# Kernel tuning notes

Measured on AMD Instinct MI355X. Metric: run time of the kernel, lower is better.

Reference implementation:

```python
import jax, jax.numpy as jnp
import numpy as np

KERNEL_SIZES = (3, 7, 15, 31)


def setup_inputs() -> dict:
    key = jax.random.key(0)
    x = jax.random.normal(key, (16, 4096, 512), dtype=jnp.float32)
    kernel_weights = jnp.ones((len(KERNEL_SIZES),), dtype=jnp.float32) / len(KERNEL_SIZES)
    return {"x": x, "kernel_weights": kernel_weights}


def _box_avg(xc, k):
    # xc: [B, F, S] channels-first; replicate-pad then depthwise box filter of width k
    B, Fc, S = xc.shape
    p = k // 2
    xp = jnp.pad(xc, ((0, 0), (0, 0), (p, p)), mode='edge')
    kern = jnp.full((Fc, 1, k), 1.0 / k, dtype=xc.dtype)  # depthwise: O=F, I/groups=1
    return jax.lax.conv_general_dilated(
        xp, kern, window_strides=(1,), padding='VALID',
        dimension_numbers=('NCW', 'OIW', 'NCW'), feature_group_count=Fc)


def reference(x, kernel_weights):
    # x: [B, S, F]
    w = jax.nn.softmax(kernel_weights)  # softmax over the 4 scales
    xc = jnp.transpose(x, (0, 2, 1))    # [B, F, S]
    out = jnp.zeros_like(xc)
    for i, k in enumerate(KERNEL_SIZES):
        out = out + w[i] * _box_avg(xc, k)
    return jnp.transpose(out, (0, 2, 1))  # [B, S, F]
```

## Files before the change

### kernel.cpp

```cpp
#include <hip/hip_runtime.h>
#include <math.h>

constexpr int B = 16;
constexpr int S = 4096;
constexpr int F = 512;
constexpr int L = 64;
constexpr int BLOCK = 256;

__global__ __launch_bounds__(BLOCK) void msavg_kernel(
    const float* __restrict__ x, const float* __restrict__ kw,
    float* __restrict__ out) {
  const int f  = blockIdx.x * BLOCK + threadIdx.x;
  const int t0 = blockIdx.y * L;
  const int b  = blockIdx.z;

  float w0 = kw[0], w1 = kw[1], w2 = kw[2], w3 = kw[3];
  float m  = fmaxf(fmaxf(w0, w1), fmaxf(w2, w3));
  float e0 = expf(w0 - m), e1 = expf(w1 - m), e2 = expf(w2 - m), e3 = expf(w3 - m);
  float inv = 1.0f / (e0 + e1 + e2 + e3);
  const float c3  = e0 * inv * (1.0f / 3.0f);
  const float c7  = e1 * inv * (1.0f / 7.0f);
  const float c15 = e2 * inv * (1.0f / 15.0f);
  const float c31 = e3 * inv * (1.0f / 31.0f);

  const float* xb = x   + ((size_t)b * S) * F + f;
  float*       ob = out + ((size_t)b * S) * F + f;

  float prev[32], cur[32];

  {
    float p = 0.0f;
#pragma unroll
    for (int j = 0; j < 32; ++j) {
      int s = t0 - 16 + j;
      s = s < 0 ? 0 : (s > S - 1 ? S - 1 : s);
      p += xb[(size_t)s * F];
      prev[j] = p;
    }
  }

#pragma unroll
  for (int g = 0; g < L / 32; ++g) {
    const int T = t0 + g * 32;

    float xv[32];
    if (T + 47 <= S - 1) {
#pragma unroll
      for (int j = 0; j < 32; ++j) xv[j] = xb[(size_t)(T + 16 + j) * F];
    } else {
#pragma unroll
      for (int j = 0; j < 32; ++j) {
        int s = T + 16 + j;
        s = s > S - 1 ? S - 1 : s;
        xv[j] = xb[(size_t)s * F];
      }
    }

    {
      float p = prev[31];
#pragma unroll
      for (int j = 0; j < 32; ++j) {
        p += xv[j];
        cur[j] = p;
      }
    }

#pragma unroll
    for (int j = 0; j < 32; ++j) {
      float Pp15 = (j < 1)  ? prev[j + 31] : cur[j - 1];
      float Pp7  = (j < 9)  ? prev[j + 23] : cur[j - 9];
      float Pp3  = (j < 13) ? prev[j + 19] : cur[j - 13];
      float Pp1  = (j < 15) ? prev[j + 17] : cur[j - 15];
      float Pm2  = (j < 18) ? prev[j + 14] : cur[j - 18];
      float Pm4  = (j < 20) ? prev[j + 12] : cur[j - 20];
      float Pm8  = (j < 24) ? prev[j + 8]  : cur[j - 24];
      float Pm16 = prev[j];
      float o = c3  * (Pp1  - Pm2) +
                c7  * (Pp3  - Pm4) +
                c15 * (Pp7  - Pm8) +
                c31 * (Pp15 - Pm16);
      ob[(size_t)(T + j) * F] = o;
    }

#pragma unroll
    for (int j = 0; j < 32; ++j) prev[j] = cur[j];
  }
}

extern "C" void kernel_launch(void* const* d_in, const int* in_sizes, int n_in,
                              void* d_out, int out_size, void* d_ws, size_t ws_size,
                              hipStream_t stream) {
  const float* x  = (const float*)d_in[0];
  const float* kw = (const float*)d_in[1];
  float* out = (float*)d_out;
  (void)in_sizes; (void)n_in; (void)out_size; (void)d_ws; (void)ws_size;

  dim3 grid(F / BLOCK, S / L, B);
  msavg_kernel<<<grid, BLOCK, 0, stream>>>(x, kw, out);
}
```

Before: 238.0 us.

## Vectorize to float2 per thread, shrink prefix window groups, add occupancy bound

Each thread now handles two adjacent feature columns using float2 vector loads and stores, and uses packed float2 arithmetic. The sliding prefix-sum window moves in 16-row groups (four groups per block) instead of 32-row groups, so fewer registers are live at once, and launch_bounds requests 4 blocks per CU. The goal is wider memory transactions and higher occupancy on this bandwidth-bound stencil. The cost is half as many blocks along F, which cuts the total thread count, and a larger register footprint per element pair that could limit the requested occupancy.

Result: slower. 265.6 us (+11.6%).

```diff
diff --git a/kernel.cpp b/kernel.cpp
--- a/kernel.cpp
+++ b/kernel.cpp
@@ -4,15 +4,20 @@
 constexpr int B = 16;
 constexpr int S = 4096;
 constexpr int F = 512;
-constexpr int L = 64;
+constexpr int G = 16;
+constexpr int NG = 4;
+constexpr int L = G * NG;
 constexpr int BLOCK = 256;
 
-__global__ __launch_bounds__(BLOCK) void msavg_kernel(
+typedef float v2f __attribute__((ext_vector_type(2)));
+static __device__ __forceinline__ v2f vs(float s) { return (v2f){s, s}; }
+
+__global__ __launch_bounds__(BLOCK, 4) void msavg_kernel(
     const float* __restrict__ x, const float* __restrict__ kw,
     float* __restrict__ out) {
-  const int f  = blockIdx.x * BLOCK + threadIdx.x;
-  const int t0 = blockIdx.y * L;
-  const int b  = blockIdx.z;
+  const int fpair = blockIdx.x * BLOCK + threadIdx.x;
+  const int t0    = blockIdx.y * L;
+  const int b     = blockIdx.z;
 
   float w0 = kw[0], w1 = kw[1], w2 = kw[2], w3 = kw[3];
   float m  = fmaxf(fmaxf(w0, w1), fmaxf(w2, w3));
@@ -23,67 +28,70 @@
   const float c15 = e2 * inv * (1.0f / 15.0f);
   const float c31 = e3 * inv * (1.0f / 31.0f);
 
-  const float* xb = x   + ((size_t)b * S) * F + f;
-  float*       ob = out + ((size_t)b * S) * F + f;
+  constexpr int RS = F / 2;
+  const v2f* xb = (const v2f*)(x   + ((size_t)b * S) * F) + fpair;
+  v2f*       ob = (v2f*)      (out + ((size_t)b * S) * F) + fpair;
 
-  float prev[32], cur[32];
-
+  v2f prev[32];
   {
-    float p = 0.0f;
+    v2f p = vs(0.0f);
 #pragma unroll
     for (int j = 0; j < 32; ++j) {
       int s = t0 - 16 + j;
       s = s < 0 ? 0 : (s > S - 1 ? S - 1 : s);
-      p += xb[(size_t)s * F];
+      p += xb[(size_t)s * RS];
       prev[j] = p;
     }
   }
 
 #pragma unroll
-  for (int g = 0; g < L / 32; ++g) {
-    const int T = t0 + g * 32;
+  for (int g = 0; g < NG; ++g) {
+    const int T = t0 + g * G;
 
-    float xv[32];
-    if (T + 47 <= S - 1) {
+    v2f xv[G];
+    if (T + 16 + G - 1 <= S - 1) {
 #pragma unroll
-      for (int j = 0; j < 32; ++j) xv[j] = xb[(size_t)(T + 16 + j) * F];
+      for (int j = 0; j < G; ++j) xv[j] = xb[(size_t)(T + 16 + j) * RS];
     } else {
 #pragma unroll
-      for (int j = 0; j < 32; ++j) {
+      for (int j = 0; j < G; ++j) {
         int s = T + 16 + j;
         s = s > S - 1 ? S - 1 : s;
-        xv[j] = xb[(size_t)s * F];
+        xv[j] = xb[(size_t)s * RS];
       }
     }
 
+    v2f cur[G];
     {
-      float p = prev[31];
+      v2f p = prev[31];
 #pragma unroll
-      for (int j = 0; j < 32; ++j) {
+      for (int j = 0; j < G; ++j) {
         p += xv[j];
         cur[j] = p;
       }
     }
 
 #pragma unroll
-    for (int j = 0; j < 32; ++j) {
-      float Pp15 = (j < 1)  ? prev[j + 31] : cur[j - 1];
-      float Pp7  = (j < 9)  ? prev[j + 23] : cur[j - 9];
-      float Pp3  = (j < 13) ? prev[j + 19] : cur[j - 13];
-      float Pp1  = (j < 15) ? prev[j + 17] : cur[j - 15];
-      float Pm2  = (j < 18) ? prev[j + 14] : cur[j - 18];
-      float Pm4  = (j < 20) ? prev[j + 12] : cur[j - 20];
-      float Pm8  = (j < 24) ? prev[j + 8]  : cur[j - 24];
-      float Pm16 = prev[j];
-      float o = c3  * (Pp1  - Pm2) +
-                c7  * (Pp3  - Pm4) +
-                c15 * (Pp7  - Pm8) +
-                c31 * (Pp15 - Pm16);
-      ob[(size_t)(T + j) * F] = o;
+    for (int j = 0; j < G; ++j) {
+      v2f Pp15 = (j < 1)  ? prev[j + 31] : cur[j - 1];
+      v2f Pp7  = (j < 9)  ? prev[j + 23] : cur[j - 9];
+      v2f Pp3  = (j < 13) ? prev[j + 19] : cur[j - 13];
+      v2f Pp1  = (j < 15) ? prev[j + 17] : cur[j - 15];
+      v2f Pm2  = prev[j + 14];
+      v2f Pm4  = prev[j + 12];
+      v2f Pm8  = prev[j + 8];
+      v2f Pm16 = prev[j];
+      v2f o = vs(c3)  * (Pp1  - Pm2) +
+              vs(c7)  * (Pp3  - Pm4) +
+              vs(c15) * (Pp7  - Pm8) +
+              vs(c31) * (Pp15 - Pm16);
+      ob[(size_t)(T + j) * RS] = o;
     }
 
 #pragma unroll
-    for (int j = 0; j < 32; ++j) prev[j] = cur[j];
+    for (int j = 0; j < 16; ++j) prev[j] = prev[j + 16];
+#pragma unroll
+    for (int j = 0; j < 16; ++j) prev[j + 16] = cur[j];
   }
 }
 
@@ -95,6 +103,6 @@
   float* out = (float*)d_out;
   (void)in_sizes; (void)n_in; (void)out_size; (void)d_ws; (void)ws_size;
 
-  dim3 grid(F / BLOCK, S / L, B);
+  dim3 grid((F / 2) / BLOCK, S / L, B);
   msavg_kernel<<<grid, BLOCK, 0, stream>>>(x, kw, out);
 }
```
